# Performance work log

Measured on AMD Instinct MI355X. Metric: run time of the kernel, lower is better.

The kernel has to match this reference:

```python
import jax, jax.numpy as jnp
import numpy as np

B, T, NIN = 32, 2048, 2
H, E, M = 256, 256, 64  # hidden, embed, attention model_dim
L = 256                  # max_output_len


def setup_inputs() -> dict:
    key = jax.random.key(0)
    ks = jax.random.split(key, 20)
    s = 0.05
    sl = jnp.sort(jax.random.randint(ks[1], (B,), 1, T + 1))[::-1]
    sl = sl.at[0].set(T)  # assert: seq_lens[0] == max_seq_len
    return {
        "sequence": jax.random.normal(ks[0], (B, T, NIN), dtype=jnp.float32),
        "seq_lens": sl.astype(jnp.int32),
        "max_output_len": L,
        # encoder input projection (Linear n_in->embed)
        "Wp": jax.random.normal(ks[2], (NIN, E)) * s,
        "bp": jnp.zeros((E,), jnp.float32),
        # encoder LSTM (torch gate order i,f,g,o)
        "W_ih_e": jax.random.normal(ks[3], (4 * H, E)) * s,
        "W_hh_e": jax.random.normal(ks[4], (4 * H, H)) * s,
        "b_ih_e": jnp.zeros((4 * H,), jnp.float32),
        "b_hh_e": jnp.zeros((4 * H,), jnp.float32),
        # decoder LSTMCell (input is previous hidden, size H)
        "W_ih_d": jax.random.normal(ks[5], (4 * H, H)) * s,
        "W_hh_d": jax.random.normal(ks[6], (4 * H, H)) * s,
        "b_ih_d": jnp.zeros((4 * H,), jnp.float32),
        "b_hh_d": jnp.zeros((4 * H,), jnp.float32),
        # scaled dot attention projections (d_q->model_dim, d_k->model_dim)
        "Wq": jax.random.normal(ks[7], (H, M)) * s,
        "bq": jnp.zeros((M,), jnp.float32),
        "Wk": jax.random.normal(ks[8], (H, M)) * s,
        "bk": jnp.zeros((M,), jnp.float32),
    }


def _lstm_cell(h, c, x, W_ih, W_hh, b_ih, b_hh):
    g = x @ W_ih.T + h @ W_hh.T + b_ih + b_hh  # [B,4H]
    i, f, gg, o = jnp.split(g, 4, axis=-1)
    c = jax.nn.sigmoid(f) * c + jax.nn.sigmoid(i) * jnp.tanh(gg)
    h = jax.nn.sigmoid(o) * jnp.tanh(c)
    return h, c


def reference(sequence, seq_lens, max_output_len, Wp, bp,
              W_ih_e, W_hh_e, b_ih_e, b_hh_e,
              W_ih_d, W_hh_d, b_ih_d, b_hh_d,
              Wq, bq, Wk, bk):
    b, t, _ = sequence.shape
    emb = sequence @ Wp + bp  # [B,T,E]

    # encoder LSTM over time (packed semantics recovered below)
    def estep(carry, x_t):
        h, c = carry
        h, c = _lstm_cell(h, c, x_t, W_ih_e, W_hh_e, b_ih_e, b_hh_e)
        return (h, c), (h, c)

    h0 = jnp.zeros((b, H), sequence.dtype)
    _, (hs, cs) = jax.lax.scan(estep, (h0, h0), emb.transpose(1, 0, 2))  # [T,B,H]

    valid = jnp.arange(t)[None, :] < seq_lens[:, None]  # [B,T]
    enc = hs.transpose(1, 0, 2) * valid[..., None]  # pad_packed zeros beyond seq_len
    bidx = jnp.arange(b)
    hT = hs[seq_lens - 1, bidx]  # final hidden at each seq's last valid step
    cT = cs[seq_lens - 1, bidx]

    # decoder: precompute K projection and mask bias (constant across steps)
    kproj = enc @ Wk + bk  # [B,T,M]
    bias = jnp.where(valid, 0.0, -1e9).astype(sequence.dtype)  # [B,T]
    scale = 1.0 / jnp.sqrt(jnp.asarray(M, sequence.dtype))

    def dstep(carry, _):
        h, c = carry
        h2, c2 = _lstm_cell(h, c, h, W_ih_d, W_hh_d, b_ih_d, b_hh_d)
        q = h2 @ Wq + bq  # [B,M]
        scores = jnp.einsum('bm,btm->bt', q, kproj) * scale + bias
        probs = jax.nn.softmax(scores, axis=-1)  # [B,T]
        return (h2, c2), probs

    _, ptrs = jax.lax.scan(dstep, (hT, cT), None, length=max_output_len)  # [L,B,T]
    return ptrs.transpose(1, 0, 2)  # [B,L,T]
```

## Files before the change

kernel.cpp:

```cpp
#include <hip/hip_runtime.h>
#include <stdint.h>

#define B_ 32
#define T_ 2048
#define H_ 256
#define M_ 64
#define L_ 256
#define G4_ 1024

#define NG_ 8
#define NSL_ 16
#define EPT_ 16
#define RING_ 8

__device__ __forceinline__ float sig_fast(float x){ return 1.f/(1.f+__expf(-x)); }
__device__ __forceinline__ float tanh_fast(float x){ return 2.f/(1.f+__expf(-2.f*x)) - 1.f; }
__device__ __forceinline__ float dot4(float4 a, float4 b){
  return fmaf(a.x,b.x, fmaf(a.y,b.y, fmaf(a.z,b.z, a.w*b.w)));
}

__global__ void prep_wdc(const float* __restrict__ a, const float* __restrict__ b,
                         float* __restrict__ o){
  int i = blockIdx.x*256 + threadIdx.x;
  o[i] = a[i] + b[i];
}

__global__ void prep_small(const float* __restrict__ Wp, const float* __restrict__ bp,
                           const float* __restrict__ Wihe, const float* __restrict__ bihe,
                           const float* __restrict__ bhhe, const float* __restrict__ bihd,
                           const float* __restrict__ bhhd, const float* __restrict__ Wq,
                           float* __restrict__ Wc0, float* __restrict__ Wc1,
                           float* __restrict__ bc, float* __restrict__ bdc,
                           float* __restrict__ WqT){
  int idx = blockIdx.x*256 + threadIdx.x;
  if (idx < 16384){
    int m = idx >> 8, k = idx & 255;
    WqT[m*256 + k] = Wq[k*64 + m];
  } else if (idx < 16384 + 1024){
    int j = idx - 16384;
    const float* wr = Wihe + j*256;
    float a0=0.f, a1=0.f, ab=0.f;
    for (int e=0;e<256;e++){
      float w = wr[e];
      a0 = fmaf(Wp[e],     w, a0);
      a1 = fmaf(Wp[256+e], w, a1);
      ab = fmaf(bp[e],     w, ab);
    }
    Wc0[j] = a0; Wc1[j] = a1;
    bc[j]  = ab + bihe[j] + bhhe[j];
    bdc[j] = bihd[j] + bhhd[j];
  }
}

__global__ __launch_bounds__(1024) void enc_kernel(
    const float* __restrict__ seq, const int* __restrict__ slen,
    const float* __restrict__ Whh,
    const float* __restrict__ Wc0, const float* __restrict__ Wc1,
    const float* __restrict__ bc,
    float* __restrict__ h_all, float* __restrict__ cT,
    unsigned long long* __restrict__ ring)
{
  const int tid = threadIdx.x;
  const int grp = blockIdx.x & 7, slice = blockIdx.x >> 3;
  const int rp = tid >> 4, kc = tid & 15;
  const int j = ((rp >> 4) << 8) + slice*EPT_ + (rp & 15);
  float4 w0 = *(const float4*)(Whh + (size_t)j*256 +   0 + kc*4);
  float4 w1 = *(const float4*)(Whh + (size_t)j*256 +  64 + kc*4);
  float4 w2 = *(const float4*)(Whh + (size_t)j*256 + 128 + kc*4);
  float4 w3 = *(const float4*)(Whh + (size_t)j*256 + 192 + kc*4);
  float c0 = Wc0[j], c1 = Wc1[j], cbv = bc[j];

  __shared__ float hbuf[4][256];
  __shared__ float sbuf[4][2];
  __shared__ float gbuf[4][64];

  const int ub = tid >> 4, ue = tid & 15;
  float creg = 0.f;
  int myb = 0, mylen = -1;
  if (tid < 64){ myb = grp + 8*ub; mylen = slen[myb]; }

  const int ib = tid >> 8, ik = tid & 255;
  unsigned long long* ringg = ring + (size_t)grp * (RING_*1024);

  for (int t = 0; t < T_; ++t){
    if (t == 0){
      hbuf[ib][ik] = 0.f;
    } else {
      const unsigned long long* pp = ringg + (size_t)((t-1) & (RING_-1))*1024 + tid;
      unsigned long long v;
      do { v = __hip_atomic_load(pp, __ATOMIC_RELAXED, __HIP_MEMORY_SCOPE_AGENT); }
      while ((unsigned)(v >> 32) != (unsigned)t);
      hbuf[ib][ik] = __uint_as_float((unsigned)v);
    }
    if (tid < 8) sbuf[tid>>1][tid&1] = seq[((size_t)(grp + 8*(tid>>1))*T_ + t)*2 + (tid&1)];
    __syncthreads();

#pragma unroll
    for (int i = 0; i < 4; ++i){
      float4 h0 = *(const float4*)&hbuf[i][       kc*4];
      float4 h1 = *(const float4*)&hbuf[i][ 64 + kc*4];
      float4 h2 = *(const float4*)&hbuf[i][128 + kc*4];
      float4 h3 = *(const float4*)&hbuf[i][192 + kc*4];
      float a = dot4(w0,h0) + dot4(w1,h1) + dot4(w2,h2) + dot4(w3,h3);
#pragma unroll
      for (int off = 1; off < 16; off <<= 1) a += __shfl_xor(a, off);
      if (kc == 0)
        gbuf[i][rp] = fmaf(sbuf[i][0], c0, fmaf(sbuf[i][1], c1, a + cbv));
    }
    __syncthreads();

    if (tid < 64){
      float gi = gbuf[ub][      ue];
      float gf = gbuf[ub][16 + ue];
      float gg = gbuf[ub][32 + ue];
      float go = gbuf[ub][48 + ue];
      creg = sig_fast(gf)*creg + sig_fast(gi)*tanh_fast(gg);
      float h = sig_fast(go)*tanh_fast(creg);
      unsigned long long pk = ((unsigned long long)(unsigned)(t+1) << 32)
                            | (unsigned long long)__float_as_uint(h);
      __hip_atomic_store(ringg + (size_t)(t & (RING_-1))*1024 + ub*256 + slice*EPT_ + ue,
                         pk, __ATOMIC_RELAXED, __HIP_MEMORY_SCOPE_AGENT);
      h_all[((size_t)t*B_ + myb)*H_ + slice*EPT_ + ue] = h;
      if (t == mylen - 1) cT[myb*H_ + slice*EPT_ + ue] = creg;
    }
  }
}

__global__ __launch_bounds__(1024) void dec_kernel(
    const int* __restrict__ slen,
    const float* __restrict__ Wdc, const float* __restrict__ bdc,
    const float* __restrict__ h_all, const float* __restrict__ cT,
    float* __restrict__ h2_all, unsigned long long* __restrict__ ring)
{
  const int tid = threadIdx.x;
  const int grp = blockIdx.x & 7, slice = blockIdx.x >> 3;
  const int rp = tid >> 4, kc = tid & 15;
  const int j = ((rp >> 4) << 8) + slice*EPT_ + (rp & 15);
  float4 w0 = *(const float4*)(Wdc + (size_t)j*256 +   0 + kc*4);
  float4 w1 = *(const float4*)(Wdc + (size_t)j*256 +  64 + kc*4);
  float4 w2 = *(const float4*)(Wdc + (size_t)j*256 + 128 + kc*4);
  float4 w3 = *(const float4*)(Wdc + (size_t)j*256 + 192 + kc*4);
  float cbv = bdc[j];

  __shared__ float hbuf[4][256];
  __shared__ float gbuf[4][64];

  const int ub = tid >> 4, ue = tid & 15;
  float creg = 0.f; int myb = 0;
  if (tid < 64){ myb = grp + 8*ub; creg = cT[myb*H_ + slice*EPT_ + ue]; }

  const int ib = tid >> 8, ik = tid & 255;
  const int stage_b = grp + 8*ib;
  const int stage_len = slen[stage_b];
  unsigned long long* ringg = ring + (size_t)grp * (RING_*1024);

  for (int s = 0; s < L_; ++s){
    if (s == 0){
      hbuf[ib][ik] = h_all[((size_t)(stage_len-1)*B_ + stage_b)*H_ + ik];
    } else {
      const unsigned long long* pp = ringg + (size_t)((s-1) & (RING_-1))*1024 + tid;
      unsigned long long v;
      do { v = __hip_atomic_load(pp, __ATOMIC_RELAXED, __HIP_MEMORY_SCOPE_AGENT); }
      while ((unsigned)(v >> 32) != (unsigned)s);
      hbuf[ib][ik] = __uint_as_float((unsigned)v);
    }
    __syncthreads();

#pragma unroll
    for (int i = 0; i < 4; ++i){
      float4 h0 = *(const float4*)&hbuf[i][       kc*4];
      float4 h1 = *(const float4*)&hbuf[i][ 64 + kc*4];
      float4 h2 = *(const float4*)&hbuf[i][128 + kc*4];
      float4 h3 = *(const float4*)&hbuf[i][192 + kc*4];
      float a = dot4(w0,h0) + dot4(w1,h1) + dot4(w2,h2) + dot4(w3,h3);
#pragma unroll
      for (int off = 1; off < 16; off <<= 1) a += __shfl_xor(a, off);
      if (kc == 0) gbuf[i][rp] = a + cbv;
    }
    __syncthreads();

    if (tid < 64){
      float gi = gbuf[ub][      ue];
      float gf = gbuf[ub][16 + ue];
      float gg = gbuf[ub][32 + ue];
      float go = gbuf[ub][48 + ue];
      creg = sig_fast(gf)*creg + sig_fast(gi)*tanh_fast(gg);
      float h = sig_fast(go)*tanh_fast(creg);
      unsigned long long pk = ((unsigned long long)(unsigned)(s+1) << 32)
                            | (unsigned long long)__float_as_uint(h);
      __hip_atomic_store(ringg + (size_t)(s & (RING_-1))*1024 + ub*256 + slice*EPT_ + ue,
                         pk, __ATOMIC_RELAXED, __HIP_MEMORY_SCOPE_AGENT);
      h2_all[((size_t)s*B_ + myb)*H_ + slice*EPT_ + ue] = h;
    }
  }
}

__global__ __launch_bounds__(256) void kproj_kernel(
    const float* __restrict__ h_all, const int* __restrict__ slen,
    const float* __restrict__ Wk, const float* __restrict__ bk,
    float* __restrict__ kp)
{
  __shared__ float wk[256*64];
  const int tid = threadIdx.x;
  const int b = blockIdx.x >> 4, tc = blockIdx.x & 15;
  const int t0 = tc*128;
#pragma unroll
  for (int i=0;i<16;i++){
    int idx = tid + i*256;
    *(float4*)(&wk[idx*4]) = *(const float4*)(Wk + idx*4);
  }
  __syncthreads();
  const int tp = tid>>2, mc = (tid&3)*16;
  const int ta = t0 + tp*2, tb = ta+1;
  const int len = slen[b];
  const bool va = ta < len, vb = tb < len;
  const float* ha = h_all + ((size_t)ta*B_ + b)*H_;
  const float* hb = h_all + ((size_t)tb*B_ + b)*H_;
  float4 A[4], Bv[4];
#pragma unroll
  for (int u=0;u<4;u++){ A[u].x=A[u].y=A[u].z=A[u].w=0.f; Bv[u]=A[u]; }

  for (int k4=0;k4<64;k4++){
    float xa[4], xb[4];
    if (va){ float4 v = *(const float4*)(ha + k4*4); xa[0]=v.x; xa[1]=v.y; xa[2]=v.z; xa[3]=v.w; }
    else   { xa[0]=xa[1]=xa[2]=xa[3]=0.f; }
    if (vb){ float4 v = *(const float4*)(hb + k4*4); xb[0]=v.x; xb[1]=v.y; xb[2]=v.z; xb[3]=v.w; }
    else   { xb[0]=xb[1]=xb[2]=xb[3]=0.f; }
#pragma unroll
    for (int jj=0;jj<4;jj++){
      const float* wr = &wk[(k4*4+jj)*64 + mc];
#pragma unroll
      for (int u=0;u<4;u++){
        float4 wv = *(const float4*)(wr + u*4);
        A[u].x  = fmaf(xa[jj],wv.x,A[u].x);  A[u].y  = fmaf(xa[jj],wv.y,A[u].y);
        A[u].z  = fmaf(xa[jj],wv.z,A[u].z);  A[u].w  = fmaf(xa[jj],wv.w,A[u].w);
        Bv[u].x = fmaf(xb[jj],wv.x,Bv[u].x); Bv[u].y = fmaf(xb[jj],wv.y,Bv[u].y);
        Bv[u].z = fmaf(xb[jj],wv.z,Bv[u].z); Bv[u].w = fmaf(xb[jj],wv.w,Bv[u].w);
      }
    }
  }
#pragma unroll
  for (int u=0;u<4;u++){
    float4 bkv = *(const float4*)(bk + mc + u*4);
    float4 ra, rb;
    ra.x = va ? A[u].x+bkv.x : bkv.x;  ra.y = va ? A[u].y+bkv.y : bkv.y;
    ra.z = va ? A[u].z+bkv.z : bkv.z;  ra.w = va ? A[u].w+bkv.w : bkv.w;
    rb.x = vb ? Bv[u].x+bkv.x : bkv.x; rb.y = vb ? Bv[u].y+bkv.y : bkv.y;
    rb.z = vb ? Bv[u].z+bkv.z : bkv.z; rb.w = vb ? Bv[u].w+bkv.w : bkv.w;
    *(float4*)(kp + ((size_t)b*T_+ta)*M_ + mc + u*4) = ra;
    *(float4*)(kp + ((size_t)b*T_+tb)*M_ + mc + u*4) = rb;
  }
}

__global__ __launch_bounds__(256) void attn_kernel(
    const float* __restrict__ h2_all, const float* __restrict__ kp,
    const float* __restrict__ WqT, const float* __restrict__ bq,
    const int* __restrict__ slen, float* __restrict__ out)
{
  const int tid = threadIdx.x;
  const int b = blockIdx.x >> 5, scg = blockIdx.x & 31;
  const int s0 = scg*8;
  __shared__ float qL[8][64];
  __shared__ float red[8][4];
  const int wid = tid>>6, lane = tid&63;

  {
    const int jj = tid>>5, mh = tid&31;
    const float* hr = h2_all + ((size_t)(s0+jj)*B_ + b)*H_;
    const float* wa = WqT + (size_t)mh*256;
    const float* wb = WqT + (size_t)(mh+32)*256;
    float a0=0.f, a1=0.f;
    for (int k4=0;k4<64;k4++){
      float4 h4 = *(const float4*)(hr + k4*4);
      float4 v0 = *(const float4*)(wa + k4*4);
      float4 v1 = *(const float4*)(wb + k4*4);
      a0 += dot4(h4,v0);
      a1 += dot4(h4,v1);
    }
    qL[jj][mh]    = a0 + bq[mh];
    qL[jj][mh+32] = a1 + bq[mh+32];
  }
  __syncthreads();

  const int len = slen[b];
  float sc_[8][8];
#pragma unroll
  for (int ti=0; ti<8; ti++){
    const int t = ti*256 + tid;
    const float* kr = kp + ((size_t)b*T_ + t)*M_;
    float tmp[8];
#pragma unroll
    for (int jj=0;jj<8;jj++) tmp[jj]=0.f;
#pragma unroll
    for (int u4=0; u4<4; u4++){
      float4 k0 = *(const float4*)(kr + u4*16);
      float4 k1 = *(const float4*)(kr + u4*16 + 4);
      float4 k2 = *(const float4*)(kr + u4*16 + 8);
      float4 k3 = *(const float4*)(kr + u4*16 + 12);
#pragma unroll
      for (int jj=0;jj<8;jj++){
        const float4* q4 = (const float4*)&qL[jj][u4*16];
        tmp[jj] += dot4(k0,q4[0]) + dot4(k1,q4[1]) + dot4(k2,q4[2]) + dot4(k3,q4[3]);
      }
    }
    float bias = (t<len) ? 0.f : -1e9f;
#pragma unroll
    for (int jj=0;jj<8;jj++) sc_[ti][jj] = fmaf(tmp[jj], 0.125f, bias);
  }

  float mx[8];
#pragma unroll
  for (int jj=0;jj<8;jj++){
    float m = sc_[0][jj];
#pragma unroll
    for (int ti=1;ti<8;ti++) m = fmaxf(m, sc_[ti][jj]);
#pragma unroll
    for (int off=1; off<64; off<<=1) m = fmaxf(m, __shfl_xor(m, off));
    if (lane==0) red[jj][wid] = m;
  }
  __syncthreads();
#pragma unroll
  for (int jj=0;jj<8;jj++)
    mx[jj] = fmaxf(fmaxf(red[jj][0],red[jj][1]), fmaxf(red[jj][2],red[jj][3]));
  __syncthreads();
#pragma unroll
  for (int jj=0;jj<8;jj++){
    float s = 0.f;
#pragma unroll
    for (int ti=0;ti<8;ti++){
      float e = __expf(sc_[ti][jj] - mx[jj]);
      sc_[ti][jj] = e;
      s += e;
    }
#pragma unroll
    for (int off=1; off<64; off<<=1) s += __shfl_xor(s, off);
    if (lane==0) red[jj][wid] = s;
  }
  __syncthreads();
#pragma unroll
  for (int jj=0;jj<8;jj++){
    float r = 1.f/(red[jj][0]+red[jj][1]+red[jj][2]+red[jj][3]);
    float* o = out + ((size_t)b*L_ + s0 + jj)*T_;
#pragma unroll
    for (int ti=0;ti<8;ti++) o[ti*256 + tid] = sc_[ti][jj]*r;
  }
}

extern "C" void kernel_launch(void* const* d_in, const int* in_sizes, int n_in,
                              void* d_out, int out_size, void* d_ws, size_t ws_size,
                              hipStream_t stream) {
  (void)in_sizes; (void)n_in; (void)out_size;
  const float* seq  = (const float*)d_in[0];
  const int*   slen = (const int*)  d_in[1];
  const float* Wp   = (const float*)d_in[3];
  const float* bp   = (const float*)d_in[4];
  const float* Wihe = (const float*)d_in[5];
  const float* Whhe = (const float*)d_in[6];
  const float* bihe = (const float*)d_in[7];
  const float* bhhe = (const float*)d_in[8];
  const float* Wihd = (const float*)d_in[9];
  const float* Whhd = (const float*)d_in[10];
  const float* bihd = (const float*)d_in[11];
  const float* bhhd = (const float*)d_in[12];
  const float* Wq   = (const float*)d_in[13];
  const float* bq   = (const float*)d_in[14];
  const float* Wk   = (const float*)d_in[15];
  const float* bk   = (const float*)d_in[16];
  float* out = (float*)d_out;

  char* p = (char*)d_ws;
  auto take = [&](size_t bytes)->char* {
    char* r = p; p += (bytes + 255) & ~(size_t)255; return r;
  };
  float* h2_all = (float*)take((size_t)L_*B_*H_*4);
  float* kproj  = (float*)take((size_t)B_*T_*M_*4);
  float* cT     = (float*)take((size_t)B_*H_*4);
  float* W_dc   = (float*)take((size_t)G4_*H_*4);
  float* Wc0    = (float*)take(G4_*4);
  float* Wc1    = (float*)take(G4_*4);
  float* bc     = (float*)take(G4_*4);
  float* b_dc   = (float*)take(G4_*4);
  float* WqT    = (float*)take((size_t)M_*H_*4);
  unsigned long long* ring_e = (unsigned long long*)take((size_t)NG_*RING_*1024*8);
  unsigned long long* ring_d = (unsigned long long*)take((size_t)NG_*RING_*1024*8);

  size_t used = (size_t)(p - (char*)d_ws);
  float* h_all;
  if (ws_size >= used + (size_t)T_*B_*H_*4) {
    h_all = (float*)take((size_t)T_*B_*H_*4);
  } else {
    h_all = out;
  }

  hipMemsetAsync(ring_e, 0, (size_t)NG_*RING_*1024*8, stream);
  hipMemsetAsync(ring_d, 0, (size_t)NG_*RING_*1024*8, stream);

  prep_wdc  <<<G4_*H_/256, 256, 0, stream>>>(Wihd, Whhd, W_dc);
  prep_small<<<68, 256, 0, stream>>>(Wp, bp, Wihe, bihe, bhhe, bihd, bhhd, Wq,
                                     Wc0, Wc1, bc, b_dc, WqT);
  enc_kernel<<<NG_*NSL_, 1024, 0, stream>>>(seq, slen, Whhe, Wc0, Wc1, bc,
                                            h_all, cT, ring_e);
  kproj_kernel<<<B_*16, 256, 0, stream>>>(h_all, slen, Wk, bk, kproj);
  dec_kernel<<<NG_*NSL_, 1024, 0, stream>>>(slen, W_dc, b_dc, h_all, cT,
                                            h2_all, ring_d);
  attn_kernel<<<B_*32, 256, 0, stream>>>(h2_all, kproj, WqT, bq, slen, out);
}
```

Before: 6.799 ms.

## Use XCD-local sc0 ring loads/stores when a block group shares one XCD

At kernel start each block reads its XCC id and publishes it, so each group can check whether all 16 slices of the recurrent LSTM ring sit on the same XCD. If they do, polling and publishing use sc0-scoped global loads and stores (L2-local) instead of agent-scope atomics, with a periodic agent-scope load as a fallback. Each block also writes its own h slice directly to shared memory and skips polling for it, and the seq load is moved before the poll. This targets the per-timestep cross-block synchronisation latency, which dominates the serial encoder and decoder loops, at the cost of relying on cache-coherence behaviour that depends on block placement.

New measurement: 20.02 ms. 194% more time.

```diff
diff --git a/kernel.cpp b/kernel.cpp
--- a/kernel.cpp
+++ b/kernel.cpp
@@ -17,6 +17,19 @@
 __device__ __forceinline__ float tanh_fast(float x){ return 2.f/(1.f+__expf(-2.f*x)) - 1.f; }
 __device__ __forceinline__ float dot4(float4 a, float4 b){
   return fmaf(a.x,b.x, fmaf(a.y,b.y, fmaf(a.z,b.z, a.w*b.w)));
+}
+
+__device__ __forceinline__ unsigned long long ld_sc0_u64(const unsigned long long* p){
+  unsigned long long r;
+  asm volatile("global_load_dwordx2 %0, %1, off sc0\n\ts_waitcnt vmcnt(0)"
+               : "=v"(r) : "v"(p) : "memory");
+  return r;
+}
+__device__ __forceinline__ void st_sc0_u64(unsigned long long* p, unsigned long long v){
+  asm volatile("global_store_dwordx2 %0, %1, off sc0" :: "v"(p), "v"(v) : "memory");
+}
+__device__ __forceinline__ unsigned long long ld_agent_u64(const unsigned long long* p){
+  return __hip_atomic_load(p, __ATOMIC_RELAXED, __HIP_MEMORY_SCOPE_AGENT);
 }
 
 __global__ void prep_wdc(const float* __restrict__ a, const float* __restrict__ b,
@@ -52,13 +65,83 @@
   }
 }
 
+template<bool FAST>
+__device__ __forceinline__ void enc_body(
+    const float* __restrict__ seq,
+    float4 w0, float4 w1, float4 w2, float4 w3,
+    float c0, float c1, float cbv,
+    float* __restrict__ h_all, float* __restrict__ cT,
+    unsigned long long* __restrict__ ringg,
+    int grp, int slice, int tid, int myb, int mylen)
+{
+  __shared__ float hbuf[4][256];
+  __shared__ float sbuf[4][2];
+  __shared__ float gbuf[4][64];
+
+  const int rp = tid >> 4, kc = tid & 15;
+  const int ub = tid >> 4, ue = tid & 15;
+  float creg = 0.f;
+
+  const int ib = tid >> 8, ik = tid & 255;
+  const bool poller = ((ik >> 4) != slice);
+
+  for (int t = 0; t < T_; ++t){
+    if (tid < 8) sbuf[tid>>1][tid&1] = seq[((size_t)(grp + 8*(tid>>1))*T_ + t)*2 + (tid&1)];
+
+    if (t == 0){
+      hbuf[ib][ik] = 0.f;
+    } else if (poller){
+      const unsigned long long* pp = ringg + (size_t)((t-1) & (RING_-1))*1024 + tid;
+      const unsigned tg = (unsigned)t;
+      unsigned long long v; unsigned r = 0;
+      do {
+        if (FAST && ((++r) & 63u)) v = ld_sc0_u64(pp);
+        else                       v = ld_agent_u64(pp);
+      } while ((unsigned)(v >> 32) != tg);
+      hbuf[ib][ik] = __uint_as_float((unsigned)v);
+    }
+    __syncthreads();
+
+#pragma unroll
+    for (int i = 0; i < 4; ++i){
+      float4 h0 = *(const float4*)&hbuf[i][       kc*4];
+      float4 h1 = *(const float4*)&hbuf[i][ 64 + kc*4];
+      float4 h2 = *(const float4*)&hbuf[i][128 + kc*4];
+      float4 h3 = *(const float4*)&hbuf[i][192 + kc*4];
+      float a = dot4(w0,h0) + dot4(w1,h1) + dot4(w2,h2) + dot4(w3,h3);
+#pragma unroll
+      for (int off = 1; off < 16; off <<= 1) a += __shfl_xor(a, off);
+      if (kc == 0)
+        gbuf[i][rp] = fmaf(sbuf[i][0], c0, fmaf(sbuf[i][1], c1, a + cbv));
+    }
+    __syncthreads();
+
+    if (tid < 64){
+      float gi = gbuf[ub][      ue];
+      float gf = gbuf[ub][16 + ue];
+      float gg = gbuf[ub][32 + ue];
+      float go = gbuf[ub][48 + ue];
+      creg = sig_fast(gf)*creg + sig_fast(gi)*tanh_fast(gg);
+      float h = sig_fast(go)*tanh_fast(creg);
+      unsigned long long pk = ((unsigned long long)(unsigned)(t+1) << 32)
+                            | (unsigned long long)__float_as_uint(h);
+      unsigned long long* dst = ringg + (size_t)(t & (RING_-1))*1024 + ub*256 + slice*EPT_ + ue;
+      if (FAST) st_sc0_u64(dst, pk);
+      else __hip_atomic_store(dst, pk, __ATOMIC_RELAXED, __HIP_MEMORY_SCOPE_AGENT);
+      hbuf[ub][slice*EPT_ + ue] = h;
+      h_all[((size_t)t*B_ + myb)*H_ + slice*EPT_ + ue] = h;
+      if (t == mylen - 1) cT[myb*H_ + slice*EPT_ + ue] = creg;
+    }
+  }
+}
+
 __global__ __launch_bounds__(1024) void enc_kernel(
     const float* __restrict__ seq, const int* __restrict__ slen,
     const float* __restrict__ Whh,
     const float* __restrict__ Wc0, const float* __restrict__ Wc1,
     const float* __restrict__ bc,
     float* __restrict__ h_all, float* __restrict__ cT,
-    unsigned long long* __restrict__ ring)
+    unsigned long long* __restrict__ ring, int* __restrict__ xb)
 {
   const int tid = threadIdx.x;
   const int grp = blockIdx.x & 7, slice = blockIdx.x >> 3;
@@ -69,30 +152,65 @@
   float4 w2 = *(const float4*)(Whh + (size_t)j*256 + 128 + kc*4);
   float4 w3 = *(const float4*)(Whh + (size_t)j*256 + 192 + kc*4);
   float c0 = Wc0[j], c1 = Wc1[j], cbv = bc[j];
-
+  int myb = 0, mylen = -1;
+  if (tid < 64){ myb = grp + 8*(tid>>4); mylen = slen[myb]; }
+  unsigned long long* ringg = ring + (size_t)grp * (RING_*1024);
+
+  int myxcd;
+  asm("s_getreg_b32 %0, hwreg(HW_REG_XCC_ID)" : "=s"(myxcd));
+  __shared__ int sfast;
+  if (tid == 0){
+    sfast = 1;
+    __hip_atomic_store(xb + grp*NSL_ + slice, myxcd + 1,
+                       __ATOMIC_RELAXED, __HIP_MEMORY_SCOPE_AGENT);
+  }
+  __syncthreads();
+  if (tid < NSL_){
+    int v;
+    do { v = __hip_atomic_load(xb + grp*NSL_ + tid,
+                               __ATOMIC_RELAXED, __HIP_MEMORY_SCOPE_AGENT); } while (v == 0);
+    if (v != myxcd + 1) sfast = 0;
+  }
+  __syncthreads();
+
+  if (sfast) enc_body<true >(seq, w0,w1,w2,w3, c0,c1,cbv, h_all, cT, ringg, grp, slice, tid, myb, mylen);
+  else       enc_body<false>(seq, w0,w1,w2,w3, c0,c1,cbv, h_all, cT, ringg, grp, slice, tid, myb, mylen);
+}
+
+template<bool FAST>
+__device__ __forceinline__ void dec_body(
+    float4 w0, float4 w1, float4 w2, float4 w3, float cbv,
+    const float* __restrict__ h_all, float* __restrict__ h2_all,
+    unsigned long long* __restrict__ ringg,
+    int grp, int slice, int tid, int myb, float creg0, int stage_len)
+{
   __shared__ float hbuf[4][256];
-  __shared__ float sbuf[4][2];
   __shared__ float gbuf[4][64];
 
+  const int rp = tid >> 4, kc = tid & 15;
   const int ub = tid >> 4, ue = tid & 15;
-  float creg = 0.f;
-  int myb = 0, mylen = -1;
-  if (tid < 64){ myb = grp + 8*ub; mylen = slen[myb]; }
-
+  float creg = creg0;
+
+  const int tb = tid >> 7, kp = tid & 127;
+  const int stage_b = grp + 8*tb;
   const int ib = tid >> 8, ik = tid & 255;
-  unsigned long long* ringg = ring + (size_t)grp * (RING_*1024);
-
-  for (int t = 0; t < T_; ++t){
-    if (t == 0){
-      hbuf[ib][ik] = 0.f;
-    } else {
-      const unsigned long long* pp = ringg + (size_t)((t-1) & (RING_-1))*1024 + tid;
-      unsigned long long v;
-      do { v = __hip_atomic_load(pp, __ATOMIC_RELAXED, __HIP_MEMORY_SCOPE_AGENT); }
-      while ((unsigned)(v >> 32) != (unsigned)t);
+  const bool poller = ((ik >> 4) != slice);
+
+  for (int s = 0; s < L_; ++s){
+    if (s == 0){
+      if (tid < 512)
+        *(float2*)&hbuf[tb][kp*2] =
+            *(const float2*)(h_all + ((size_t)(stage_len-1)*B_ + stage_b)*H_ + kp*2);
+    } else if (poller){
+      const unsigned long long* pp = ringg + (size_t)((s-1) & (RING_-1))*1024 + tid;
+      const unsigned tg = (unsigned)s;
+      unsigned long long v; unsigned r = 0;
+      do {
+        if (FAST && ((++r) & 63u)) v = ld_sc0_u64(pp);
+        else                       v = ld_agent_u64(pp);
+      } while ((unsigned)(v >> 32) != tg);
       hbuf[ib][ik] = __uint_as_float((unsigned)v);
     }
-    if (tid < 8) sbuf[tid>>1][tid&1] = seq[((size_t)(grp + 8*(tid>>1))*T_ + t)*2 + (tid&1)];
     __syncthreads();
 
 #pragma unroll
@@ -104,8 +222,7 @@
       float a = dot4(w0,h0) + dot4(w1,h1) + dot4(w2,h2) + dot4(w3,h3);
 #pragma unroll
       for (int off = 1; off < 16; off <<= 1) a += __shfl_xor(a, off);
-      if (kc == 0)
-        gbuf[i][rp] = fmaf(sbuf[i][0], c0, fmaf(sbuf[i][1], c1, a + cbv));
+      if (kc == 0) gbuf[i][rp] = a + cbv;
     }
     __syncthreads();
 
@@ -116,12 +233,13 @@
       float go = gbuf[ub][48 + ue];
       creg = sig_fast(gf)*creg + sig_fast(gi)*tanh_fast(gg);
       float h = sig_fast(go)*tanh_fast(creg);
-      unsigned long long pk = ((unsigned long long)(unsigned)(t+1) << 32)
+      unsigned long long pk = ((unsigned long long)(unsigned)(s+1) << 32)
                             | (unsigned long long)__float_as_uint(h);
-      __hip_atomic_store(ringg + (size_t)(t & (RING_-1))*1024 + ub*256 + slice*EPT_ + ue,
-                         pk, __ATOMIC_RELAXED, __HIP_MEMORY_SCOPE_AGENT);
-      h_all[((size_t)t*B_ + myb)*H_ + slice*EPT_ + ue] = h;
-      if (t == mylen - 1) cT[myb*H_ + slice*EPT_ + ue] = creg;
+      unsigned long long* dst = ringg + (size_t)(s & (RING_-1))*1024 + ub*256 + slice*EPT_ + ue;
+      if (FAST) st_sc0_u64(dst, pk);
+      else __hip_atomic_store(dst, pk, __ATOMIC_RELAXED, __HIP_MEMORY_SCOPE_AGENT);
+      hbuf[ub][slice*EPT_ + ue] = h;
+      h2_all[((size_t)s*B_ + myb)*H_ + slice*EPT_ + ue] = h;
     }
   }
 }
@@ -130,7 +248,8 @@
     const int* __restrict__ slen,
     const float* __restrict__ Wdc, const float* __restrict__ bdc,
     const float* __restrict__ h_all, const float* __restrict__ cT,
-    float* __restrict__ h2_all, unsigned long long* __restrict__ ring)
+    float* __restrict__ h2_all,
+    unsigned long long* __restrict__ ring, int* __restrict__ xb)
 {
   const int tid = threadIdx.x;
   const int grp = blockIdx.x & 7, slice = blockIdx.x >> 3;
@@ -141,58 +260,31 @@
   float4 w2 = *(const float4*)(Wdc + (size_t)j*256 + 128 + kc*4);
   float4 w3 = *(const float4*)(Wdc + (size_t)j*256 + 192 + kc*4);
   float cbv = bdc[j];
-
-  __shared__ float hbuf[4][256];
-  __shared__ float gbuf[4][64];
-
-  const int ub = tid >> 4, ue = tid & 15;
-  float creg = 0.f; int myb = 0;
-  if (tid < 64){ myb = grp + 8*ub; creg = cT[myb*H_ + slice*EPT_ + ue]; }
-
-  const int ib = tid >> 8, ik = tid & 255;
-  const int stage_b = grp + 8*ib;
-  const int stage_len = slen[stage_b];
+  int myb = 0; float creg0 = 0.f;
+  if (tid < 64){ myb = grp + 8*(tid>>4); creg0 = cT[myb*H_ + slice*EPT_ + (tid&15)]; }
+  int stage_len = 1;
+  if (tid < 512) stage_len = slen[grp + 8*(tid>>7)];
   unsigned long long* ringg = ring + (size_t)grp * (RING_*1024);
 
-  for (int s = 0; s < L_; ++s){
-    if (s == 0){
-      hbuf[ib][ik] = h_all[((size_t)(stage_len-1)*B_ + stage_b)*H_ + ik];
-    } else {
-      const unsigned long long* pp = ringg + (size_t)((s-1) & (RING_-1))*1024 + tid;
-      unsigned long long v;
-      do { v = __hip_atomic_load(pp, __ATOMIC_RELAXED, __HIP_MEMORY_SCOPE_AGENT); }
-      while ((unsigned)(v >> 32) != (unsigned)s);
-      hbuf[ib][ik] = __uint_as_float((unsigned)v);
-    }
-    __syncthreads();
-
-#pragma unroll
-    for (int i = 0; i < 4; ++i){
-      float4 h0 = *(const float4*)&hbuf[i][       kc*4];
-      float4 h1 = *(const float4*)&hbuf[i][ 64 + kc*4];
-      float4 h2 = *(const float4*)&hbuf[i][128 + kc*4];
-      float4 h3 = *(const float4*)&hbuf[i][192 + kc*4];
-      float a = dot4(w0,h0) + dot4(w1,h1) + dot4(w2,h2) + dot4(w3,h3);
-#pragma unroll
-      for (int off = 1; off < 16; off <<= 1) a += __shfl_xor(a, off);
-      if (kc == 0) gbuf[i][rp] = a + cbv;
-    }
-    __syncthreads();
-
-    if (tid < 64){
-      float gi = gbuf[ub][      ue];
-      float gf = gbuf[ub][16 + ue];
-      float gg = gbuf[ub][32 + ue];
-      float go = gbuf[ub][48 + ue];
-      creg = sig_fast(gf)*creg + sig_fast(gi)*tanh_fast(gg);
-      float h = sig_fast(go)*tanh_fast(creg);
-      unsigned long long pk = ((unsigned long long)(unsigned)(s+1) << 32)
-                            | (unsigned long long)__float_as_uint(h);
-      __hip_atomic_store(ringg + (size_t)(s & (RING_-1))*1024 + ub*256 + slice*EPT_ + ue,
-                         pk, __ATOMIC_RELAXED, __HIP_MEMORY_SCOPE_AGENT);
-      h2_all[((size_t)s*B_ + myb)*H_ + slice*EPT_ + ue] = h;
-    }
-  }
+  int myxcd;
+  asm("s_getreg_b32 %0, hwreg(HW_REG_XCC_ID)" : "=s"(myxcd));
+  __shared__ int sfast;
+  if (tid == 0){
+    sfast = 1;
+    __hip_atomic_store(xb + grp*NSL_ + slice, myxcd + 1,
+                       __ATOMIC_RELAXED, __HIP_MEMORY_SCOPE_AGENT);
+  }
+  __syncthreads();
+  if (tid < NSL_){
+    int v;
+    do { v = __hip_atomic_load(xb + grp*NSL_ + tid,
+                               __ATOMIC_RELAXED, __HIP_MEMORY_SCOPE_AGENT); } while (v == 0);
+    if (v != myxcd + 1) sfast = 0;
+  }
+  __syncthreads();
+
+  if (sfast) dec_body<true >(w0,w1,w2,w3, cbv, h_all, h2_all, ringg, grp, slice, tid, myb, creg0, stage_len);
+  else       dec_body<false>(w0,w1,w2,w3, cbv, h_all, h2_all, ringg, grp, slice, tid, myb, creg0, stage_len);
 }
 
 __global__ __launch_bounds__(256) void kproj_kernel(
@@ -221,11 +313,11 @@
   for (int u=0;u<4;u++){ A[u].x=A[u].y=A[u].z=A[u].w=0.f; Bv[u]=A[u]; }
 
   for (int k4=0;k4<64;k4++){
-    float xa[4], xb[4];
+    float xa[4], xb_[4];
     if (va){ float4 v = *(const float4*)(ha + k4*4); xa[0]=v.x; xa[1]=v.y; xa[2]=v.z; xa[3]=v.w; }
     else   { xa[0]=xa[1]=xa[2]=xa[3]=0.f; }
-    if (vb){ float4 v = *(const float4*)(hb + k4*4); xb[0]=v.x; xb[1]=v.y; xb[2]=v.z; xb[3]=v.w; }
-    else   { xb[0]=xb[1]=xb[2]=xb[3]=0.f; }
+    if (vb){ float4 v = *(const float4*)(hb + k4*4); xb_[0]=v.x; xb_[1]=v.y; xb_[2]=v.z; xb_[3]=v.w; }
+    else   { xb_[0]=xb_[1]=xb_[2]=xb_[3]=0.f; }
 #pragma unroll
     for (int jj=0;jj<4;jj++){
       const float* wr = &wk[(k4*4+jj)*64 + mc];
@@ -234,8 +326,8 @@
         float4 wv = *(const float4*)(wr + u*4);
         A[u].x  = fmaf(xa[jj],wv.x,A[u].x);  A[u].y  = fmaf(xa[jj],wv.y,A[u].y);
         A[u].z  = fmaf(xa[jj],wv.z,A[u].z);  A[u].w  = fmaf(xa[jj],wv.w,A[u].w);
-        Bv[u].x = fmaf(xb[jj],wv.x,Bv[u].x); Bv[u].y = fmaf(xb[jj],wv.y,Bv[u].y);
-        Bv[u].z = fmaf(xb[jj],wv.z,Bv[u].z); Bv[u].w = fmaf(xb[jj],wv.w,Bv[u].w);
+        Bv[u].x = fmaf(xb_[jj],wv.x,Bv[u].x); Bv[u].y = fmaf(xb_[jj],wv.y,Bv[u].y);
+        Bv[u].z = fmaf(xb_[jj],wv.z,Bv[u].z); Bv[u].w = fmaf(xb_[jj],wv.w,Bv[u].w);
       }
     }
   }
@@ -383,6 +475,8 @@
   float* WqT    = (float*)take((size_t)M_*H_*4);
   unsigned long long* ring_e = (unsigned long long*)take((size_t)NG_*RING_*1024*8);
   unsigned long long* ring_d = (unsigned long long*)take((size_t)NG_*RING_*1024*8);
+  int* xb_e = (int*)take((size_t)NG_*NSL_*4);
+  int* xb_d = (int*)take((size_t)NG_*NSL_*4);
 
   size_t used = (size_t)(p - (char*)d_ws);
   float* h_all;
@@ -394,14 +488,16 @@
 
   hipMemsetAsync(ring_e, 0, (size_t)NG_*RING_*1024*8, stream);
   hipMemsetAsync(ring_d, 0, (size_t)NG_*RING_*1024*8, stream);
+  hipMemsetAsync(xb_e,   0, (size_t)NG_*NSL_*4, stream);
+  hipMemsetAsync(xb_d,   0, (size_t)NG_*NSL_*4, stream);
 
   prep_wdc  <<<G4_*H_/256, 256, 0, stream>>>(Wihd, Whhd, W_dc);
   prep_small<<<68, 256, 0, stream>>>(Wp, bp, Wihe, bihe, bhhe, bihd, bhhd, Wq,
                                      Wc0, Wc1, bc, b_dc, WqT);
   enc_kernel<<<NG_*NSL_, 1024, 0, stream>>>(seq, slen, Whhe, Wc0, Wc1, bc,
-                                            h_all, cT, ring_e);
+                                            h_all, cT, ring_e, xb_e);
   kproj_kernel<<<B_*16, 256, 0, stream>>>(h_all, slen, Wk, bk, kproj);
   dec_kernel<<<NG_*NSL_, 1024, 0, stream>>>(slen, W_dc, b_dc, h_all, cT,
-                                            h2_all, ring_d);
+                                            h2_all, ring_d, xb_d);
   attn_kernel<<<B_*32, 256, 0, stream>>>(h2_all, kproj, WqT, bq, slen, out);
 }
```

## Restructure LSTM recurrence to one barrier per step with thread-local gate fusion

Applied to the files above, without the earlier changes.

Each thread group now computes all four gates for one hidden unit and batch, so the gate nonlinearities run in registers right after the shuffle reduction. This removes the gbuf shared-memory round trip and one of the two __syncthreads per timestep. The h buffer is double-buffered, the block writes its own slice of h directly into local shared memory instead of polling the ring for it, and the next step's input is prefetched. The cost is four times as many weight registers per thread (64 floats), which may raise register pressure.

New measurement: 7.656 ms. 12.6% more time.

```diff
diff --git a/kernel.cpp b/kernel.cpp
--- a/kernel.cpp
+++ b/kernel.cpp
@@ -17,6 +17,9 @@
 __device__ __forceinline__ float tanh_fast(float x){ return 2.f/(1.f+__expf(-2.f*x)) - 1.f; }
 __device__ __forceinline__ float dot4(float4 a, float4 b){
   return fmaf(a.x,b.x, fmaf(a.y,b.y, fmaf(a.z,b.z, a.w*b.w)));
+}
+__device__ __forceinline__ unsigned long long ld_ag(const unsigned long long* p){
+  return __hip_atomic_load(p, __ATOMIC_RELAXED, __HIP_MEMORY_SCOPE_AGENT);
 }
 
 __global__ void prep_wdc(const float* __restrict__ a, const float* __restrict__ b,
@@ -62,67 +65,82 @@
 {
   const int tid = threadIdx.x;
   const int grp = blockIdx.x & 7, slice = blockIdx.x >> 3;
-  const int rp = tid >> 4, kc = tid & 15;
-  const int j = ((rp >> 4) << 8) + slice*EPT_ + (rp & 15);
-  float4 w0 = *(const float4*)(Whh + (size_t)j*256 +   0 + kc*4);
-  float4 w1 = *(const float4*)(Whh + (size_t)j*256 +  64 + kc*4);
-  float4 w2 = *(const float4*)(Whh + (size_t)j*256 + 128 + kc*4);
-  float4 w3 = *(const float4*)(Whh + (size_t)j*256 + 192 + kc*4);
-  float c0 = Wc0[j], c1 = Wc1[j], cbv = bc[j];
-
-  __shared__ float hbuf[4][256];
-  __shared__ float sbuf[4][2];
-  __shared__ float gbuf[4][64];
-
-  const int ub = tid >> 4, ue = tid & 15;
+  const int kc = tid & 15, gid = tid >> 4;
+  const int ib = gid >> 4, ue = gid & 15;
+  const int hofs = slice*EPT_ + ue;
+  const int myb = grp + 8*ib;
+  const int mylen = slen[myb];
+
+  float4 wv[4][4];
+#pragma unroll
+  for (int g=0; g<4; ++g){
+    const float* wr = Whh + (size_t)(g*256 + hofs)*256;
+#pragma unroll
+    for (int u=0; u<4; ++u) wv[g][u] = *(const float4*)(wr + u*64 + kc*4);
+  }
+  float c0g[4], c1g[4], cbg[4];
+#pragma unroll
+  for (int g=0; g<4; ++g){
+    int j = g*256 + hofs;
+    c0g[g] = Wc0[j]; c1g[g] = Wc1[j]; cbg[g] = bc[j];
+  }
   float creg = 0.f;
-  int myb = 0, mylen = -1;
-  if (tid < 64){ myb = grp + 8*ub; mylen = slen[myb]; }
-
-  const int ib = tid >> 8, ik = tid & 255;
+
+  __shared__ float hbuf[2][4][256];
+  __shared__ float sbuf[2][4][2];
+  const int pib = tid >> 8, pik = tid & 255;
+  const bool pol = ((pik >> 4) != slice);
   unsigned long long* ringg = ring + (size_t)grp * (RING_*1024);
 
+  hbuf[0][pib][pik] = 0.f;
+  if (tid < 8) sbuf[0][tid>>1][tid&1] = seq[((size_t)(grp + 8*(tid>>1))*T_ + 0)*2 + (tid&1)];
+  __syncthreads();
+
   for (int t = 0; t < T_; ++t){
-    if (t == 0){
-      hbuf[ib][ik] = 0.f;
-    } else {
-      const unsigned long long* pp = ringg + (size_t)((t-1) & (RING_-1))*1024 + tid;
-      unsigned long long v;
-      do { v = __hip_atomic_load(pp, __ATOMIC_RELAXED, __HIP_MEMORY_SCOPE_AGENT); }
-      while ((unsigned)(v >> 32) != (unsigned)t);
-      hbuf[ib][ik] = __uint_as_float((unsigned)v);
-    }
-    if (tid < 8) sbuf[tid>>1][tid&1] = seq[((size_t)(grp + 8*(tid>>1))*T_ + t)*2 + (tid&1)];
-    __syncthreads();
-
-#pragma unroll
-    for (int i = 0; i < 4; ++i){
-      float4 h0 = *(const float4*)&hbuf[i][       kc*4];
-      float4 h1 = *(const float4*)&hbuf[i][ 64 + kc*4];
-      float4 h2 = *(const float4*)&hbuf[i][128 + kc*4];
-      float4 h3 = *(const float4*)&hbuf[i][192 + kc*4];
-      float a = dot4(w0,h0) + dot4(w1,h1) + dot4(w2,h2) + dot4(w3,h3);
-#pragma unroll
-      for (int off = 1; off < 16; off <<= 1) a += __shfl_xor(a, off);
-      if (kc == 0)
-        gbuf[i][rp] = fmaf(sbuf[i][0], c0, fmaf(sbuf[i][1], c1, a + cbv));
-    }
-    __syncthreads();
-
-    if (tid < 64){
-      float gi = gbuf[ub][      ue];
-      float gf = gbuf[ub][16 + ue];
-      float gg = gbuf[ub][32 + ue];
-      float go = gbuf[ub][48 + ue];
+    const int cur = t & 1;
+    if (tid < 8 && t+1 < T_)
+      sbuf[cur^1][tid>>1][tid&1] = seq[((size_t)(grp + 8*(tid>>1))*T_ + (t+1))*2 + (tid&1)];
+
+    float4 h4[4];
+#pragma unroll
+    for (int u=0; u<4; ++u) h4[u] = *(const float4*)&hbuf[cur][ib][u*64 + kc*4];
+    float a0 = dot4(wv[0][0],h4[0]) + dot4(wv[0][1],h4[1]) + dot4(wv[0][2],h4[2]) + dot4(wv[0][3],h4[3]);
+    float a1 = dot4(wv[1][0],h4[0]) + dot4(wv[1][1],h4[1]) + dot4(wv[1][2],h4[2]) + dot4(wv[1][3],h4[3]);
+    float a2 = dot4(wv[2][0],h4[0]) + dot4(wv[2][1],h4[1]) + dot4(wv[2][2],h4[2]) + dot4(wv[2][3],h4[3]);
+    float a3 = dot4(wv[3][0],h4[0]) + dot4(wv[3][1],h4[1]) + dot4(wv[3][2],h4[2]) + dot4(wv[3][3],h4[3]);
+#pragma unroll
+    for (int off = 1; off < 16; off <<= 1){
+      a0 += __shfl_xor(a0, off);
+      a1 += __shfl_xor(a1, off);
+      a2 += __shfl_xor(a2, off);
+      a3 += __shfl_xor(a3, off);
+    }
+
+    if (kc == 0){
+      float s0 = sbuf[cur][ib][0], s1 = sbuf[cur][ib][1];
+      float gi = fmaf(s0,c0g[0], fmaf(s1,c1g[0], a0 + cbg[0]));
+      float gf = fmaf(s0,c0g[1], fmaf(s1,c1g[1], a1 + cbg[1]));
+      float gg = fmaf(s0,c0g[2], fmaf(s1,c1g[2], a2 + cbg[2]));
+      float go = fmaf(s0,c0g[3], fmaf(s1,c1g[3], a3 + cbg[3]));
       creg = sig_fast(gf)*creg + sig_fast(gi)*tanh_fast(gg);
       float h = sig_fast(go)*tanh_fast(creg);
       unsigned long long pk = ((unsigned long long)(unsigned)(t+1) << 32)
                             | (unsigned long long)__float_as_uint(h);
-      __hip_atomic_store(ringg + (size_t)(t & (RING_-1))*1024 + ub*256 + slice*EPT_ + ue,
+      __hip_atomic_store(ringg + (size_t)(t & (RING_-1))*1024 + ib*256 + hofs,
                          pk, __ATOMIC_RELAXED, __HIP_MEMORY_SCOPE_AGENT);
-      h_all[((size_t)t*B_ + myb)*H_ + slice*EPT_ + ue] = h;
-      if (t == mylen - 1) cT[myb*H_ + slice*EPT_ + ue] = creg;
-    }
+      hbuf[cur^1][ib][hofs] = h;
+      h_all[((size_t)t*B_ + myb)*H_ + hofs] = h;
+      if (t == mylen - 1) cT[myb*H_ + hofs] = creg;
+    }
+
+    if (t+1 < T_ && pol){
+      const unsigned long long* pp = ringg + (size_t)(t & (RING_-1))*1024 + tid;
+      const unsigned tg = (unsigned)(t+1);
+      unsigned long long v;
+      do { v = ld_ag(pp); } while ((unsigned)(v >> 32) != tg);
+      hbuf[cur^1][pib][pik] = __uint_as_float((unsigned)v);
+    }
+    __syncthreads();
   }
 }
 
@@ -134,64 +152,71 @@
 {
   const int tid = threadIdx.x;
   const int grp = blockIdx.x & 7, slice = blockIdx.x >> 3;
-  const int rp = tid >> 4, kc = tid & 15;
-  const int j = ((rp >> 4) << 8) + slice*EPT_ + (rp & 15);
-  float4 w0 = *(const float4*)(Wdc + (size_t)j*256 +   0 + kc*4);
-  float4 w1 = *(const float4*)(Wdc + (size_t)j*256 +  64 + kc*4);
-  float4 w2 = *(const float4*)(Wdc + (size_t)j*256 + 128 + kc*4);
-  float4 w3 = *(const float4*)(Wdc + (size_t)j*256 + 192 + kc*4);
-  float cbv = bdc[j];
-
-  __shared__ float hbuf[4][256];
-  __shared__ float gbuf[4][64];
-
-  const int ub = tid >> 4, ue = tid & 15;
-  float creg = 0.f; int myb = 0;
-  if (tid < 64){ myb = grp + 8*ub; creg = cT[myb*H_ + slice*EPT_ + ue]; }
-
-  const int ib = tid >> 8, ik = tid & 255;
-  const int stage_b = grp + 8*ib;
-  const int stage_len = slen[stage_b];
+  const int kc = tid & 15, gid = tid >> 4;
+  const int ib = gid >> 4, ue = gid & 15;
+  const int hofs = slice*EPT_ + ue;
+  const int myb = grp + 8*ib;
+
+  float4 wv[4][4];
+#pragma unroll
+  for (int g=0; g<4; ++g){
+    const float* wr = Wdc + (size_t)(g*256 + hofs)*256;
+#pragma unroll
+    for (int u=0; u<4; ++u) wv[g][u] = *(const float4*)(wr + u*64 + kc*4);
+  }
+  float cbg[4];
+#pragma unroll
+  for (int g=0; g<4; ++g) cbg[g] = bdc[g*256 + hofs];
+  float creg = cT[myb*H_ + hofs];
+
+  __shared__ float hbuf[2][4][256];
+  const int pib = tid >> 8, pik = tid & 255;
+  const bool pol = ((pik >> 4) != slice);
   unsigned long long* ringg = ring + (size_t)grp * (RING_*1024);
 
+  {
+    const int blen = slen[grp + 8*pib];
+    hbuf[0][pib][pik] = h_all[((size_t)(blen-1)*B_ + (grp + 8*pib))*H_ + pik];
+  }
+  __syncthreads();
+
   for (int s = 0; s < L_; ++s){
-    if (s == 0){
-      hbuf[ib][ik] = h_all[((size_t)(stage_len-1)*B_ + stage_b)*H_ + ik];
-    } else {
-      const unsigned long long* pp = ringg + (size_t)((s-1) & (RING_-1))*1024 + tid;
-      unsigned long long v;
-      do { v = __hip_atomic_load(pp, __ATOMIC_RELAXED, __HIP_MEMORY_SCOPE_AGENT); }
-      while ((unsigned)(v >> 32) != (unsigned)s);
-      hbuf[ib][ik] = __uint_as_float((unsigned)v);
-    }
-    __syncthreads();
-
-#pragma unroll
-    for (int i = 0; i < 4; ++i){
-      float4 h0 = *(const float4*)&hbuf[i][       kc*4];
-      float4 h1 = *(const float4*)&hbuf[i][ 64 + kc*4];
-      float4 h2 = *(const float4*)&hbuf[i][128 + kc*4];
-      float4 h3 = *(const float4*)&hbuf[i][192 + kc*4];
-      float a = dot4(w0,h0) + dot4(w1,h1) + dot4(w2,h2) + dot4(w3,h3);
-#pragma unroll
-      for (int off = 1; off < 16; off <<= 1) a += __shfl_xor(a, off);
-      if (kc == 0) gbuf[i][rp] = a + cbv;
-    }
-    __syncthreads();
-
-    if (tid < 64){
-      float gi = gbuf[ub][      ue];
-      float gf = gbuf[ub][16 + ue];
-      float gg = gbuf[ub][32 + ue];
-      float go = gbuf[ub][48 + ue];
+    const int cur = s & 1;
+    float4 h4[4];
+#pragma unroll
+    for (int u=0; u<4; ++u) h4[u] = *(const float4*)&hbuf[cur][ib][u*64 + kc*4];
+    float a0 = dot4(wv[0][0],h4[0]) + dot4(wv[0][1],h4[1]) + dot4(wv[0][2],h4[2]) + dot4(wv[0][3],h4[3]);
+    float a1 = dot4(wv[1][0],h4[0]) + dot4(wv[1][1],h4[1]) + dot4(wv[1][2],h4[2]) + dot4(wv[1][3],h4[3]);
+    float a2 = dot4(wv[2][0],h4[0]) + dot4(wv[2][1],h4[1]) + dot4(wv[2][2],h4[2]) + dot4(wv[2][3],h4[3]);
+    float a3 = dot4(wv[3][0],h4[0]) + dot4(wv[3][1],h4[1]) + dot4(wv[3][2],h4[2]) + dot4(wv[3][3],h4[3]);
+#pragma unroll
+    for (int off = 1; off < 16; off <<= 1){
+      a0 += __shfl_xor(a0, off);
+      a1 += __shfl_xor(a1, off);
+      a2 += __shfl_xor(a2, off);
+      a3 += __shfl_xor(a3, off);
+    }
+
+    if (kc == 0){
+      float gi = a0 + cbg[0], gf = a1 + cbg[1], gg = a2 + cbg[2], go = a3 + cbg[3];
       creg = sig_fast(gf)*creg + sig_fast(gi)*tanh_fast(gg);
       float h = sig_fast(go)*tanh_fast(creg);
       unsigned long long pk = ((unsigned long long)(unsigned)(s+1) << 32)
                             | (unsigned long long)__float_as_uint(h);
-      __hip_atomic_store(ringg + (size_t)(s & (RING_-1))*1024 + ub*256 + slice*EPT_ + ue,
+      __hip_atomic_store(ringg + (size_t)(s & (RING_-1))*1024 + ib*256 + hofs,
                          pk, __ATOMIC_RELAXED, __HIP_MEMORY_SCOPE_AGENT);
-      h2_all[((size_t)s*B_ + myb)*H_ + slice*EPT_ + ue] = h;
-    }
+      hbuf[cur^1][ib][hofs] = h;
+      h2_all[((size_t)s*B_ + myb)*H_ + hofs] = h;
+    }
+
+    if (s+1 < L_ && pol){
+      const unsigned long long* pp = ringg + (size_t)(s & (RING_-1))*1024 + tid;
+      const unsigned tg = (unsigned)(s+1);
+      unsigned long long v;
+      do { v = ld_ag(pp); } while ((unsigned)(v >> 32) != tg);
+      hbuf[cur^1][pib][pik] = __uint_as_float((unsigned)v);
+    }
+    __syncthreads();
   }
 }
 
@@ -221,11 +246,11 @@
   for (int u=0;u<4;u++){ A[u].x=A[u].y=A[u].z=A[u].w=0.f; Bv[u]=A[u]; }
 
   for (int k4=0;k4<64;k4++){
-    float xa[4], xb[4];
+    float xa[4], xb_[4];
     if (va){ float4 v = *(const float4*)(ha + k4*4); xa[0]=v.x; xa[1]=v.y; xa[2]=v.z; xa[3]=v.w; }
     else   { xa[0]=xa[1]=xa[2]=xa[3]=0.f; }
-    if (vb){ float4 v = *(const float4*)(hb + k4*4); xb[0]=v.x; xb[1]=v.y; xb[2]=v.z; xb[3]=v.w; }
-    else   { xb[0]=xb[1]=xb[2]=xb[3]=0.f; }
+    if (vb){ float4 v = *(const float4*)(hb + k4*4); xb_[0]=v.x; xb_[1]=v.y; xb_[2]=v.z; xb_[3]=v.w; }
+    else   { xb_[0]=xb_[1]=xb_[2]=xb_[3]=0.f; }
 #pragma unroll
     for (int jj=0;jj<4;jj++){
       const float* wr = &wk[(k4*4+jj)*64 + mc];
@@ -234,8 +259,8 @@
         float4 wv = *(const float4*)(wr + u*4);
         A[u].x  = fmaf(xa[jj],wv.x,A[u].x);  A[u].y  = fmaf(xa[jj],wv.y,A[u].y);
         A[u].z  = fmaf(xa[jj],wv.z,A[u].z);  A[u].w  = fmaf(xa[jj],wv.w,A[u].w);
-        Bv[u].x = fmaf(xb[jj],wv.x,Bv[u].x); Bv[u].y = fmaf(xb[jj],wv.y,Bv[u].y);
-        Bv[u].z = fmaf(xb[jj],wv.z,Bv[u].z); Bv[u].w = fmaf(xb[jj],wv.w,Bv[u].w);
+        Bv[u].x = fmaf(xb_[jj],wv.x,Bv[u].x); Bv[u].y = fmaf(xb_[jj],wv.y,Bv[u].y);
+        Bv[u].z = fmaf(xb_[jj],wv.z,Bv[u].z); Bv[u].w = fmaf(xb_[jj],wv.w,Bv[u].w);
       }
     }
   }
```
